# Performance work log

Hardware: AMD Instinct MI355X
Metric: run time of the kernel (lower is better)

The kernel has to match this reference:

```python
import jax, jax.numpy as jnp
import numpy as np

N_NODES = 20000
N_EDGES = 320000
IN_CH = 256
HID_CH = 256   # 2 * out_channels
OUT_CH = 128


def gcn_conv(x, edge_index, W, b, n_nodes):
    """PyG GCNConv: linear transform, add self-loops, sym-normalized scatter-add."""
    x = x @ W  # [N, C_out]
    loop = jnp.arange(n_nodes, dtype=edge_index.dtype)
    row = jnp.concatenate([edge_index[0], loop])  # source nodes
    col = jnp.concatenate([edge_index[1], loop])  # destination nodes
    deg = jax.ops.segment_sum(jnp.ones_like(col, dtype=x.dtype), col,
                              num_segments=n_nodes)
    deg_inv_sqrt = jnp.where(deg > 0, jax.lax.rsqrt(deg), 0.0)
    norm = deg_inv_sqrt[row] * deg_inv_sqrt[col]  # [E+N]
    msg = x[row] * norm[:, None]                  # gather + scale
    out = jax.ops.segment_sum(msg, col, num_segments=n_nodes)  # scatter-add
    return out + b


def setup_inputs() -> dict:
    key = jax.random.key(0)
    k1, k2, k3, k4, k5 = jax.random.split(key, 5)
    doc_embeds = jax.random.normal(k1, (N_NODES, IN_CH), dtype=jnp.float32)
    edge_index = jax.random.randint(k2, (2, N_EDGES), 0, N_NODES, dtype=jnp.int64)
    # Glorot-style init for GCN weights, zero bias (PyG defaults)
    s1 = 1.0 / np.sqrt(IN_CH)
    s2 = 1.0 / np.sqrt(HID_CH)
    W1 = jax.random.uniform(k3, (IN_CH, HID_CH), jnp.float32, -s1, s1)
    b1 = jnp.zeros((HID_CH,), jnp.float32)
    W2 = jax.random.uniform(k4, (HID_CH, OUT_CH), jnp.float32, -s2, s2)
    b2 = jnp.zeros((OUT_CH,), jnp.float32)
    return {"doc_embeds": doc_embeds, "edge_index": edge_index,
            "W1": W1, "b1": b1, "W2": W2, "b2": b2}


def reference(doc_embeds, edge_index, W1, b1, W2, b2):
    n = doc_embeds.shape[0]
    x = jax.nn.relu(gcn_conv(doc_embeds, edge_index, W1, b1, n))
    x = gcn_conv(x, edge_index, W2, b2, n)
    return x
```

## Files before the change

### kernel.cpp

```cpp
#include <hip/hip_runtime.h>
#include <math.h>

#define N_NODES 20000
#define N_EDGES 320000
#define IN_CH   256
#define HID_CH  256
#define OUT_CH  128
#define CAP     64
#define GK      256

typedef __attribute__((ext_vector_type(8))) unsigned short ushort8;
typedef __attribute__((ext_vector_type(4))) unsigned short ushort4v;
typedef __attribute__((ext_vector_type(4))) float floatx4;
typedef __attribute__((ext_vector_type(2))) float floatx2;
typedef __attribute__((ext_vector_type(2))) _Float16 half2v;
typedef __attribute__((ext_vector_type(8))) _Float16 half8;

__global__ __launch_bounds__(256)
void prep_kernel(const float* __restrict__ W1, const float* __restrict__ W2,
                 _Float16* __restrict__ W1t, _Float16* __restrict__ W2t,
                 const int* __restrict__ row, const int* __restrict__ col,
                 int* __restrict__ deg, unsigned short* __restrict__ srcs) {
    const int g = blockIdx.x * blockDim.x + threadIdx.x;
    const int gsz = gridDim.x * blockDim.x;
    for (int t = g; t < (IN_CH * HID_CH) / 16; t += gsz) {
        int n = t >> 4;
        int kc = (t & 15) * 16;
        half8 h0, h1;
#pragma unroll
        for (int j = 0; j < 8; ++j) {
            h0[j] = (_Float16)W1[(size_t)(kc + j) * HID_CH + n];
            h1[j] = (_Float16)W1[(size_t)(kc + 8 + j) * HID_CH + n];
        }
        *(half8*)(W1t + (size_t)n * IN_CH + kc)     = h0;
        *(half8*)(W1t + (size_t)n * IN_CH + kc + 8) = h1;
    }
    for (int t = g; t < (HID_CH * OUT_CH) / 16; t += gsz) {
        int n = t >> 4;
        int kc = (t & 15) * 16;
        half8 h0, h1;
#pragma unroll
        for (int j = 0; j < 8; ++j) {
            h0[j] = (_Float16)W2[(size_t)(kc + j) * OUT_CH + n];
            h1[j] = (_Float16)W2[(size_t)(kc + 8 + j) * OUT_CH + n];
        }
        *(half8*)(W2t + (size_t)n * HID_CH + kc)     = h0;
        *(half8*)(W2t + (size_t)n * HID_CH + kc + 8) = h1;
    }
    for (int i = g; i < N_EDGES; i += gsz) {
        int c = col[i];
        int r = row[i];
        int p = atomicAdd(&deg[c], 1);
        srcs[(size_t)c * CAP + p] = (unsigned short)r;
    }
}

template <int AMODE, int TN>
__global__ __launch_bounds__(256, 2)
void gemm_mfma_kernel(const float* __restrict__ Afp, const _Float16* __restrict__ Ah,
                      const _Float16* __restrict__ Bt,
                      const int* __restrict__ deg, _Float16* __restrict__ C, int M, int N) {
    constexpr int NJ = TN / 32;
    __shared__ _Float16 As[64][36];
    __shared__ _Float16 Bs[TN][36];
    const int tid = threadIdx.x;
    const int m0 = blockIdx.y * 64;
    const int n0 = blockIdx.x * TN;
    const int lane = tid & 63;
    const int wave = tid >> 6;
    const int wr = (wave >> 1) * 32;
    const int wc = (wave & 1) * (TN / 2);
    const int lm = lane & 15;
    const int lk = (lane >> 4) * 8;

    floatx4 acc[2][NJ];
#pragma unroll
    for (int i = 0; i < 2; ++i)
#pragma unroll
        for (int j = 0; j < NJ; ++j) acc[i][j] = (floatx4){0.f, 0.f, 0.f, 0.f};

    const int ar  = tid >> 2;
    const int ako = (tid & 3) * 8;

    for (int k0 = 0; k0 < GK; k0 += 32) {
        {
            half8 va = {};
            if (m0 + ar < M) {
                if (AMODE == 1) {
                    const float* ap = Afp + (size_t)(m0 + ar) * GK + k0 + ako;
                    float4 f0 = *(const float4*)ap;
                    float4 f1 = *(const float4*)(ap + 4);
                    va[0] = (_Float16)f0.x; va[1] = (_Float16)f0.y;
                    va[2] = (_Float16)f0.z; va[3] = (_Float16)f0.w;
                    va[4] = (_Float16)f1.x; va[5] = (_Float16)f1.y;
                    va[6] = (_Float16)f1.z; va[7] = (_Float16)f1.w;
                } else {
                    va = *(const half8*)(Ah + (size_t)(m0 + ar) * GK + k0 + ako);
                }
            }
            *(half8*)&As[ar][ako] = va;
        }
#pragma unroll
        for (int c = 0; c < TN / 64; ++c) {
            int ch = tid + c * 256;
            int r  = ch >> 2;
            int ko = (ch & 3) * 8;
            *(half8*)&Bs[r][ko] = *(const half8*)(Bt + (size_t)(n0 + r) * GK + k0 + ko);
        }
        __syncthreads();

        half8 ah[2];
#pragma unroll
        for (int i = 0; i < 2; ++i)
            ah[i] = *(const half8*)&As[wr + i * 16 + lm][lk];
#pragma unroll
        for (int j = 0; j < NJ; ++j) {
            half8 bh = *(const half8*)&Bs[wc + j * 16 + lm][lk];
#pragma unroll
            for (int i = 0; i < 2; ++i)
                acc[i][j] = __builtin_amdgcn_mfma_f32_16x16x32_f16(ah[i], bh, acc[i][j], 0, 0, 0);
        }
        __syncthreads();
    }

#pragma unroll
    for (int i = 0; i < 2; ++i) {
#pragma unroll
        for (int r = 0; r < 4; ++r) {
            int rowi = m0 + wr + i * 16 + (lane >> 4) * 4 + r;
            if (rowi < M) {
                float dr = 1.0f / sqrtf((float)(deg[rowi] + 1));
#pragma unroll
                for (int j = 0; j < NJ; ++j) {
                    C[(size_t)rowi * N + n0 + wc + j * 16 + lm] = (_Float16)(dr * acc[i][j][r]);
                }
            }
        }
    }
}

template <int C, int NSLICE, int MODE>
__global__ __launch_bounds__(256)
void gather_sliced_kernel(const _Float16* __restrict__ X, const int* __restrict__ deg,
                          const unsigned short* __restrict__ srcs,
                          const float* __restrict__ bias, float* __restrict__ outf,
                          _Float16* __restrict__ outh, int n) {
    constexpr int SW = C / NSLICE;
    static_assert(SW == 32, "slice must be 32 channels");
    const int slice = blockIdx.x % NSLICE;
    const int ngrp  = blockIdx.x / NSLICE;
    const int wave = threadIdx.x >> 6;
    const int lane = threadIdx.x & 63;
    const int g  = lane >> 4;
    const int sl = lane & 15;
    const int node = ngrp * 16 + wave * 4 + g;
    if (node >= n) return;
    const int choff = slice * SW + sl * 2;
    const size_t beg = (size_t)node * CAP;
    const int cnt = deg[node];

    float a0 = 0.f, a1 = 0.f;
    int e = 0;
    for (; e + 8 <= cnt; e += 8) {
        ushort8 s8 = *(const ushort8*)(srcs + beg + e);
        half2v v0 = *(const half2v*)(X + (size_t)s8[0] * C + choff);
        half2v v1 = *(const half2v*)(X + (size_t)s8[1] * C + choff);
        half2v v2 = *(const half2v*)(X + (size_t)s8[2] * C + choff);
        half2v v3 = *(const half2v*)(X + (size_t)s8[3] * C + choff);
        half2v v4 = *(const half2v*)(X + (size_t)s8[4] * C + choff);
        half2v v5 = *(const half2v*)(X + (size_t)s8[5] * C + choff);
        half2v v6 = *(const half2v*)(X + (size_t)s8[6] * C + choff);
        half2v v7 = *(const half2v*)(X + (size_t)s8[7] * C + choff);
        a0 += (float)v0.x + (float)v1.x + (float)v2.x + (float)v3.x
            + (float)v4.x + (float)v5.x + (float)v6.x + (float)v7.x;
        a1 += (float)v0.y + (float)v1.y + (float)v2.y + (float)v3.y
            + (float)v4.y + (float)v5.y + (float)v6.y + (float)v7.y;
    }
    for (; e + 4 <= cnt; e += 4) {
        ushort4v s4 = *(const ushort4v*)(srcs + beg + e);
        half2v v0 = *(const half2v*)(X + (size_t)s4.x * C + choff);
        half2v v1 = *(const half2v*)(X + (size_t)s4.y * C + choff);
        half2v v2 = *(const half2v*)(X + (size_t)s4.z * C + choff);
        half2v v3 = *(const half2v*)(X + (size_t)s4.w * C + choff);
        a0 += (float)v0.x + (float)v1.x + (float)v2.x + (float)v3.x;
        a1 += (float)v0.y + (float)v1.y + (float)v2.y + (float)v3.y;
    }
    for (; e < cnt; ++e) {
        int r = srcs[beg + e];
        half2v v = *(const half2v*)(X + (size_t)r * C + choff);
        a0 += (float)v.x; a1 += (float)v.y;
    }

    const float dc = 1.0f / sqrtf((float)(cnt + 1));
    half2v vsh = *(const half2v*)(X + (size_t)node * C + choff);
    float2 bb = *(const float2*)(bias + choff);

    float o0 = dc * (a0 + (float)vsh.x) + bb.x;
    float o1 = dc * (a1 + (float)vsh.y) + bb.y;

    if constexpr (MODE == 1) {
        half2v h;
        h.x = (_Float16)fmaxf(o0, 0.f);
        h.y = (_Float16)fmaxf(o1, 0.f);
        *(half2v*)(outh + (size_t)node * C + choff) = h;
    } else {
        floatx2 o = {o0, o1};
        __builtin_nontemporal_store(o, (floatx2*)(outf + (size_t)node * C + choff));
    }
}

extern "C" void kernel_launch(void* const* d_in, const int* in_sizes, int n_in,
                              void* d_out, int out_size, void* d_ws, size_t ws_size,
                              hipStream_t stream) {
    const float* doc_embeds = (const float*)d_in[0];
    const int*   edge_index = (const int*)d_in[1];
    const float* W1 = (const float*)d_in[2];
    const float* b1 = (const float*)d_in[3];
    const float* W2 = (const float*)d_in[4];
    const float* b2 = (const float*)d_in[5];
    float* out = (float*)d_out;

    const int* row = edge_index;
    const int* col = edge_index + N_EDGES;

    char* ws = (char*)d_ws;
    auto align_up = [](size_t x) { return (x + 255) / 256 * 256; };

    _Float16* X1s = (_Float16*)(ws);
    _Float16* H1  = (_Float16*)(ws + align_up((size_t)N_NODES * HID_CH * 2));
    _Float16* X2s = X1s;
    char* meta = (char*)(ws + 2 * align_up((size_t)N_NODES * HID_CH * 2));
    _Float16* W1t = (_Float16*)(meta); meta += align_up((size_t)IN_CH * HID_CH * 2);
    _Float16* W2t = (_Float16*)(meta); meta += align_up((size_t)HID_CH * OUT_CH * 2);
    int*            deg  = (int*)(meta);            meta += align_up((size_t)N_NODES * 4);
    unsigned short* srcs = (unsigned short*)(meta);

    hipMemsetAsync(deg, 0, (size_t)N_NODES * 4, stream);
    prep_kernel<<<(N_EDGES + 255) / 256, 256, 0, stream>>>(
        W1, W2, W1t, W2t, row, col, deg, srcs);

    {
        dim3 grid(HID_CH / 128, (N_NODES + 63) / 64);
        gemm_mfma_kernel<1, 128><<<grid, 256, 0, stream>>>(
            doc_embeds, nullptr, W1t, deg, X1s, N_NODES, HID_CH);
    }
    gather_sliced_kernel<HID_CH, 8, 1><<<((N_NODES + 15) / 16) * 8, 256, 0, stream>>>(
        X1s, deg, srcs, b1, nullptr, H1, N_NODES);

    {
        dim3 grid(OUT_CH / 128, (N_NODES + 63) / 64);
        gemm_mfma_kernel<2, 128><<<grid, 256, 0, stream>>>(
            nullptr, H1, W2t, deg, X2s, N_NODES, OUT_CH);
    }
    gather_sliced_kernel<OUT_CH, 4, 0><<<((N_NODES + 15) / 16) * 4, 256, 0, stream>>>(
        X2s, deg, srcs, b2, out, nullptr, N_NODES);
}
```

Before: 165.3 us.

## Fuse layer-1 aggregation into the layer-2 GEMM A-tile load

Drops the separate layer-1 gather kernel and the H1 intermediate buffer. The second GEMM now builds its A tile on the fly: each thread gathers 8 channels of its node's neighbors from X1s, applies normalization, bias and ReLU, and writes the result into shared memory. This saves one launch and the H1 write and read-back. In exchange, the gather now runs with only 313 blocks, one per 64 rows, and each thread walks the neighbor list serially inside the K loop, so latency hiding and parallelism for the gather drop.

```diff
diff --git a/kernel.cpp b/kernel.cpp
--- a/kernel.cpp
+++ b/kernel.cpp
@@ -55,29 +55,26 @@
     }
 }
 
-template <int AMODE, int TN>
 __global__ __launch_bounds__(256, 2)
-void gemm_mfma_kernel(const float* __restrict__ Afp, const _Float16* __restrict__ Ah,
-                      const _Float16* __restrict__ Bt,
-                      const int* __restrict__ deg, _Float16* __restrict__ C, int M, int N) {
-    constexpr int NJ = TN / 32;
+void gemm1_kernel(const float* __restrict__ Afp, const _Float16* __restrict__ Bt,
+                  const int* __restrict__ deg, _Float16* __restrict__ C, int M, int N) {
     __shared__ _Float16 As[64][36];
-    __shared__ _Float16 Bs[TN][36];
+    __shared__ _Float16 Bs[128][36];
     const int tid = threadIdx.x;
     const int m0 = blockIdx.y * 64;
-    const int n0 = blockIdx.x * TN;
+    const int n0 = blockIdx.x * 128;
     const int lane = tid & 63;
     const int wave = tid >> 6;
     const int wr = (wave >> 1) * 32;
-    const int wc = (wave & 1) * (TN / 2);
+    const int wc = (wave & 1) * 64;
     const int lm = lane & 15;
     const int lk = (lane >> 4) * 8;
 
-    floatx4 acc[2][NJ];
+    floatx4 acc[2][4];
 #pragma unroll
     for (int i = 0; i < 2; ++i)
 #pragma unroll
-        for (int j = 0; j < NJ; ++j) acc[i][j] = (floatx4){0.f, 0.f, 0.f, 0.f};
+        for (int j = 0; j < 4; ++j) acc[i][j] = (floatx4){0.f, 0.f, 0.f, 0.f};
 
     const int ar  = tid >> 2;
     const int ako = (tid & 3) * 8;
@@ -86,22 +83,18 @@
         {
             half8 va = {};
             if (m0 + ar < M) {
-                if (AMODE == 1) {
-                    const float* ap = Afp + (size_t)(m0 + ar) * GK + k0 + ako;
-                    float4 f0 = *(const float4*)ap;
-                    float4 f1 = *(const float4*)(ap + 4);
-                    va[0] = (_Float16)f0.x; va[1] = (_Float16)f0.y;
-                    va[2] = (_Float16)f0.z; va[3] = (_Float16)f0.w;
-                    va[4] = (_Float16)f1.x; va[5] = (_Float16)f1.y;
-                    va[6] = (_Float16)f1.z; va[7] = (_Float16)f1.w;
-                } else {
-                    va = *(const half8*)(Ah + (size_t)(m0 + ar) * GK + k0 + ako);
-                }
+                const float* ap = Afp + (size_t)(m0 + ar) * GK + k0 + ako;
+                float4 f0 = *(const float4*)ap;
+                float4 f1 = *(const float4*)(ap + 4);
+                va[0] = (_Float16)f0.x; va[1] = (_Float16)f0.y;
+                va[2] = (_Float16)f0.z; va[3] = (_Float16)f0.w;
+                va[4] = (_Float16)f1.x; va[5] = (_Float16)f1.y;
+                va[6] = (_Float16)f1.z; va[7] = (_Float16)f1.w;
             }
             *(half8*)&As[ar][ako] = va;
         }
 #pragma unroll
-        for (int c = 0; c < TN / 64; ++c) {
+        for (int c = 0; c < 2; ++c) {
             int ch = tid + c * 256;
             int r  = ch >> 2;
             int ko = (ch & 3) * 8;
@@ -114,7 +107,7 @@
         for (int i = 0; i < 2; ++i)
             ah[i] = *(const half8*)&As[wr + i * 16 + lm][lk];
 #pragma unroll
-        for (int j = 0; j < NJ; ++j) {
+        for (int j = 0; j < 4; ++j) {
             half8 bh = *(const half8*)&Bs[wc + j * 16 + lm][lk];
 #pragma unroll
             for (int i = 0; i < 2; ++i)
@@ -131,7 +124,7 @@
             if (rowi < M) {
                 float dr = 1.0f / sqrtf((float)(deg[rowi] + 1));
 #pragma unroll
-                for (int j = 0; j < NJ; ++j) {
+                for (int j = 0; j < 4; ++j) {
                     C[(size_t)rowi * N + n0 + wc + j * 16 + lm] = (_Float16)(dr * acc[i][j][r]);
                 }
             }
@@ -139,12 +132,113 @@
     }
 }
 
-template <int C, int NSLICE, int MODE>
+__global__ __launch_bounds__(256, 2)
+void gemm2_fused_kernel(const _Float16* __restrict__ X, const int* __restrict__ deg,
+                        const unsigned short* __restrict__ srcs,
+                        const float* __restrict__ b1, const _Float16* __restrict__ Bt,
+                        _Float16* __restrict__ C) {
+    __shared__ _Float16 As[64][36];
+    __shared__ _Float16 Bs[128][36];
+    const int tid = threadIdx.x;
+    const int m0 = blockIdx.x * 64;
+    const int lane = tid & 63;
+    const int wave = tid >> 6;
+    const int wr = (wave >> 1) * 32;
+    const int wc = (wave & 1) * 64;
+    const int lm = lane & 15;
+    const int lk = (lane >> 4) * 8;
+
+    const int ar  = tid >> 2;
+    const int ako = (tid & 3) * 8;
+    const int node = m0 + ar;
+    const bool valid = node < N_NODES;
+    const int cnt = valid ? deg[node] : 0;
+    const float dc = 1.0f / sqrtf((float)(cnt + 1));
+    const size_t beg = (size_t)node * CAP;
+
+    floatx4 acc[2][4];
+#pragma unroll
+    for (int i = 0; i < 2; ++i)
+#pragma unroll
+        for (int j = 0; j < 4; ++j) acc[i][j] = (floatx4){0.f, 0.f, 0.f, 0.f};
+
+    for (int k0 = 0; k0 < GK; k0 += 32) {
+        {
+            const _Float16* Xb = X + k0 + ako;
+            float a[8] = {0.f, 0.f, 0.f, 0.f, 0.f, 0.f, 0.f, 0.f};
+            int e = 0;
+            for (; e + 4 <= cnt; e += 4) {
+                ushort4v s4 = *(const ushort4v*)(srcs + beg + e);
+                half8 v0 = *(const half8*)(Xb + (size_t)s4.x * GK);
+                half8 v1 = *(const half8*)(Xb + (size_t)s4.y * GK);
+                half8 v2 = *(const half8*)(Xb + (size_t)s4.z * GK);
+                half8 v3 = *(const half8*)(Xb + (size_t)s4.w * GK);
+#pragma unroll
+                for (int j = 0; j < 8; ++j)
+                    a[j] += (float)v0[j] + (float)v1[j] + (float)v2[j] + (float)v3[j];
+            }
+            for (; e < cnt; ++e) {
+                int r = srcs[beg + e];
+                half8 v = *(const half8*)(Xb + (size_t)r * GK);
+#pragma unroll
+                for (int j = 0; j < 8; ++j) a[j] += (float)v[j];
+            }
+            half8 hv = {};
+            if (valid) {
+                half8 self = *(const half8*)(Xb + (size_t)node * GK);
+                float4 bb0 = *(const float4*)(b1 + k0 + ako);
+                float4 bb1 = *(const float4*)(b1 + k0 + ako + 4);
+                float bj[8] = {bb0.x, bb0.y, bb0.z, bb0.w, bb1.x, bb1.y, bb1.z, bb1.w};
+#pragma unroll
+                for (int j = 0; j < 8; ++j)
+                    hv[j] = (_Float16)fmaxf(dc * (a[j] + (float)self[j]) + bj[j], 0.f);
+            }
+            *(half8*)&As[ar][ako] = hv;
+        }
+#pragma unroll
+        for (int c = 0; c < 2; ++c) {
+            int ch = tid + c * 256;
+            int r  = ch >> 2;
+            int ko = (ch & 3) * 8;
+            *(half8*)&Bs[r][ko] = *(const half8*)(Bt + (size_t)r * GK + k0 + ko);
+        }
+        __syncthreads();
+
+        half8 ah[2];
+#pragma unroll
+        for (int i = 0; i < 2; ++i)
+            ah[i] = *(const half8*)&As[wr + i * 16 + lm][lk];
+#pragma unroll
+        for (int j = 0; j < 4; ++j) {
+            half8 bh = *(const half8*)&Bs[wc + j * 16 + lm][lk];
+#pragma unroll
+            for (int i = 0; i < 2; ++i)
+                acc[i][j] = __builtin_amdgcn_mfma_f32_16x16x32_f16(ah[i], bh, acc[i][j], 0, 0, 0);
+        }
+        __syncthreads();
+    }
+
+#pragma unroll
+    for (int i = 0; i < 2; ++i) {
+#pragma unroll
+        for (int r = 0; r < 4; ++r) {
+            int rowi = m0 + wr + i * 16 + (lane >> 4) * 4 + r;
+            if (rowi < N_NODES) {
+                float dr = 1.0f / sqrtf((float)(deg[rowi] + 1));
+#pragma unroll
+                for (int j = 0; j < 4; ++j) {
+                    C[(size_t)rowi * OUT_CH + wc + j * 16 + lm] = (_Float16)(dr * acc[i][j][r]);
+                }
+            }
+        }
+    }
+}
+
+template <int C, int NSLICE>
 __global__ __launch_bounds__(256)
-void gather_sliced_kernel(const _Float16* __restrict__ X, const int* __restrict__ deg,
-                          const unsigned short* __restrict__ srcs,
-                          const float* __restrict__ bias, float* __restrict__ outf,
-                          _Float16* __restrict__ outh, int n) {
+void gather_out_kernel(const _Float16* __restrict__ X, const int* __restrict__ deg,
+                       const unsigned short* __restrict__ srcs,
+                       const float* __restrict__ bias, float* __restrict__ outf, int n) {
     constexpr int SW = C / NSLICE;
     static_assert(SW == 32, "slice must be 32 channels");
     const int slice = blockIdx.x % NSLICE;
@@ -198,15 +292,8 @@
     float o0 = dc * (a0 + (float)vsh.x) + bb.x;
     float o1 = dc * (a1 + (float)vsh.y) + bb.y;
 
-    if constexpr (MODE == 1) {
-        half2v h;
-        h.x = (_Float16)fmaxf(o0, 0.f);
-        h.y = (_Float16)fmaxf(o1, 0.f);
-        *(half2v*)(outh + (size_t)node * C + choff) = h;
-    } else {
-        floatx2 o = {o0, o1};
-        __builtin_nontemporal_store(o, (floatx2*)(outf + (size_t)node * C + choff));
-    }
+    floatx2 o = {o0, o1};
+    __builtin_nontemporal_store(o, (floatx2*)(outf + (size_t)node * C + choff));
 }
 
 extern "C" void kernel_launch(void* const* d_in, const int* in_sizes, int n_in,
@@ -227,8 +314,7 @@
     auto align_up = [](size_t x) { return (x + 255) / 256 * 256; };
 
     _Float16* X1s = (_Float16*)(ws);
-    _Float16* H1  = (_Float16*)(ws + align_up((size_t)N_NODES * HID_CH * 2));
-    _Float16* X2s = X1s;
+    _Float16* X2s = (_Float16*)(ws + align_up((size_t)N_NODES * HID_CH * 2));
     char* meta = (char*)(ws + 2 * align_up((size_t)N_NODES * HID_CH * 2));
     _Float16* W1t = (_Float16*)(meta); meta += align_up((size_t)IN_CH * HID_CH * 2);
     _Float16* W2t = (_Float16*)(meta); meta += align_up((size_t)HID_CH * OUT_CH * 2);
@@ -241,17 +327,13 @@
 
     {
         dim3 grid(HID_CH / 128, (N_NODES + 63) / 64);
-        gemm_mfma_kernel<1, 128><<<grid, 256, 0, stream>>>(
-            doc_embeds, nullptr, W1t, deg, X1s, N_NODES, HID_CH);
-    }
-    gather_sliced_kernel<HID_CH, 8, 1><<<((N_NODES + 15) / 16) * 8, 256, 0, stream>>>(
-        X1s, deg, srcs, b1, nullptr, H1, N_NODES);
-
-    {
-        dim3 grid(OUT_CH / 128, (N_NODES + 63) / 64);
-        gemm_mfma_kernel<2, 128><<<grid, 256, 0, stream>>>(
-            nullptr, H1, W2t, deg, X2s, N_NODES, OUT_CH);
-    }
-    gather_sliced_kernel<OUT_CH, 4, 0><<<((N_NODES + 15) / 16) * 4, 256, 0, stream>>>(
-        X2s, deg, srcs, b2, out, nullptr, N_NODES);
-}
+        gemm1_kernel<<<grid, 256, 0, stream>>>(
+            doc_embeds, W1t, deg, X1s, N_NODES, HID_CH);
+    }
+
+    gemm2_fused_kernel<<<(N_NODES + 63) / 64, 256, 0, stream>>>(
+        X1s, deg, srcs, b1, W2t, X2s);
+
+    gather_out_kernel<OUT_CH, 4><<<((N_NODES + 15) / 16) * 4, 256, 0, stream>>>(
+        X2s, deg, srcs, b2, out, N_NODES);
+}
```

Measured after the change: 183.9 us. +11.2%, slower.
